# Kernel optimization log

Hardware: AMD Instinct MI355X
Metric: run time of the kernel (lower is better)

Reference implementation:

```python
import jax, jax.numpy as jnp
import numpy as np

B = 4        # samples
GP = 6       # graphs per sample (K*2)
N = 1024     # nodes per graph
DIN = 128    # input feature dim
D = 128      # out_channels
E = 16384    # edges per graph


def setup_inputs() -> dict:
    k = jax.random.split(jax.random.key(0), 10)
    G = B * GP
    s = 0.05
    return {
        "x": jax.random.normal(k[0], (G, N, DIN), jnp.float32),
        "edge_attr": jax.random.uniform(k[1], (G, E, 6), jnp.float32),
        "gcn_W": jax.random.normal(k[2], (4, DIN, D), jnp.float32) * s,
        "gcn_b": jnp.zeros((4, D), jnp.float32),
        "Ws": jax.random.normal(k[3], (4, D, D), jnp.float32) * s,
        "lin1_W": jax.random.normal(k[4], (GP * D, 20), jnp.float32) * s,
        "lin1_b": jnp.zeros((20,), jnp.float32),
        "codefc_W": jax.random.normal(k[5], (20, 2), jnp.float32) * s,
        "codefc_b": jnp.zeros((2,), jnp.float32),
        "lin2_W": jax.random.normal(k[6], (GP * D, GP), jnp.float32) * s,
        "lin2_b": jnp.zeros((GP,), jnp.float32),
        "simfc_W": jax.random.normal(k[7], (GP, 2), jnp.float32) * s,
        "simfc_b": jnp.zeros((2,), jnp.float32),
        "edge_index": jax.random.randint(k[8], (G, 2, E), 0, N, jnp.int64),
    }


def _gcn(x, src, dst, ew, W, b):
    # PyG GCNConv with normalize=True, add_self_loops=True (self-loop weight 1)
    n = x.shape[0]
    deg = jax.ops.segment_sum(ew, dst, num_segments=n) + 1.0
    dinv = jax.lax.rsqrt(deg)
    xw = x @ W
    norm = dinv[src] * ew * dinv[dst]               # [E]
    agg = jax.ops.segment_sum(norm[:, None] * xw[src], dst, num_segments=n)
    return agg + (dinv * dinv)[:, None] * xw + b    # self-loop term + bias


def _gnnlayer(x, ei, ea, gcn_W, gcn_b, Ws):
    # x_tmp = sum_i relu(GCN_i(x, ew=edge_attr[:, i+2])) @ Ws[i]
    src, dst = ei[0], ei[1]
    def chan(W, b, Wmix, ew):
        return jnp.maximum(_gcn(x, src, dst, ew, W, b), 0.0) @ Wmix
    return jax.vmap(chan)(gcn_W, gcn_b, Ws, ea[:, 2:6].T).sum(0)  # [N, D]


def _forward(x, edge_attr, gcn_W, gcn_b, Ws, lin1_W, lin1_b, codefc_W,
             codefc_b, lin2_W, lin2_b, simfc_W, simfc_b, edge_index):
    # per-graph GNN layer over all G = B*GP graphs
    x_tmp = jax.vmap(lambda xg, eig, eag: _gnnlayer(xg, eig, eag, gcn_W, gcn_b, Ws))(
        x, edge_index, edge_attr)                    # [G, N, D]
    g = x_tmp.mean(axis=1).reshape(B, GP * D)        # g_matrix [B, 768]
    # L2-normalize rows (F.normalize eps=1e-12)
    xn = x_tmp / jnp.clip(jnp.linalg.norm(x_tmp, axis=-1, keepdims=True), 1e-12)
    xn = xn.reshape(B, GP, N, D)
    # all-pairs cosine sim -> tanh -> 21-bin histogram on [-1, 1] -> weighted sum
    S = jnp.tanh(jnp.einsum('bind,bjmd->bijnm', xn, xn))   # [B,GP,GP,N,N]
    idx = jnp.clip(jnp.floor((S + 1.0) * (21.0 / 2.0)).astype(jnp.int32), 0, 20)
    centers = jnp.linspace(-1.0, 1.0, 21, dtype=jnp.float32)
    # hist/(N*N) dot centers == mean of per-element bin centers
    sim = centers[idx].mean(axis=(3, 4))             # [B, GP, GP]
    # backnet
    feat = jnp.maximum(g @ lin1_W + lin1_b, 0.0)     # feature_of_G [B, 20]
    code = jax.nn.log_softmax(feat @ codefc_W + codefc_b, axis=1)
    strength = g @ lin2_W + lin2_b                   # [B, GP]
    sim_res = jax.nn.log_softmax((sim.mean(axis=2) * strength) @ simfc_W + simfc_b, axis=1)
    r = 0.4 * code + 0.6 * sim_res
    return r, feat


def reference(x, edge_attr, gcn_W, gcn_b, Ws, lin1_W, lin1_b, codefc_W,
              codefc_b, lin2_W, lin2_b, simfc_W, simfc_b, edge_index):
    return _forward(x, edge_attr, gcn_W, gcn_b, Ws, lin1_W, lin1_b, codefc_W,
                    codefc_b, lin2_W, lin2_b, simfc_W, simfc_b, edge_index)
```

## Files before the change

### kernel.cpp

```cpp
#include <hip/hip_runtime.h>

#define NG 24
#define NB 4
#define GPg 6
#define NN 1024
#define DD 128
#define EE 16384

typedef __bf16 bf16;
typedef __bf16 bf16x8 __attribute__((ext_vector_type(8)));
typedef float f32x4 __attribute__((ext_vector_type(4)));

#define GLOBAL_AS __attribute__((address_space(1)))
#define LDS_AS __attribute__((address_space(3)))

__device__ __forceinline__ int binidx(float v) {
  float u = v * v;
  float q = fmaf(fmaf(fmaf(-0.261093f, u, 1.222977f), u, -3.463278f), u, 10.49874f);
  return (int)fmaf(v, q, 10.5f);
}

__global__ void k_histw(const int* __restrict__ ei, int* __restrict__ counts,
                        const float* __restrict__ gW, const float* __restrict__ Ws,
                        bf16* __restrict__ gwt, bf16* __restrict__ wst) {
  int bid = blockIdx.x;
  if (bid >= 1536) {
    int i = (bid - 1536) * 256 + threadIdx.x;
    int c = i >> 14, k = (i >> 7) & 127, j = i & 127;
    gwt[(c << 14) | (j << 7) | k] = (bf16)gW[i];
    wst[(j << 9) | (c << 7) | k] = (bf16)Ws[i];
    return;
  }
  int t = bid * 256 + threadIdx.x;
  int g = t >> 14, e = t & (EE - 1);
  int dst = ei[g * 2 * EE + EE + e];
  atomicAdd(&counts[g * NN + dst], 1);
}

__global__ void k_scan(const int* __restrict__ counts, int* __restrict__ offs,
                       int* __restrict__ cursor) {
  __shared__ int sh[NN];
  int g = blockIdx.x, t = threadIdx.x;
  int myc = counts[g * NN + t];
  sh[t] = myc;
  __syncthreads();
  for (int d2 = 1; d2 < NN; d2 <<= 1) {
    int v = (t >= d2) ? sh[t - d2] : 0;
    __syncthreads();
    sh[t] += v;
    __syncthreads();
  }
  int incl = sh[t];
  int excl = incl - myc;
  offs[g * 1025 + t] = excl;
  cursor[g * NN + t] = excl;
  if (t == NN - 1) offs[g * 1025 + NN] = incl;
}

__global__ void k_scatter(const int* __restrict__ ei, const float* __restrict__ ea,
                          int* __restrict__ cursor, int* __restrict__ csrs,
                          float* __restrict__ csre) {
  int t = blockIdx.x * 256 + threadIdx.x;
  if (t >= NG * EE) return;
  int g = t >> 14, e = t & (EE - 1);
  int src = ei[g * 2 * EE + e], dst = ei[g * 2 * EE + EE + e];
  int pos = atomicAdd(&cursor[g * NN + dst], 1);
  size_t idx = (size_t)g * EE + pos;
  csrs[idx] = src;
  const float* p = ea + ((size_t)g * EE + e) * 6;
  float2 q0 = *(const float2*)(p + 2);
  float2 q1 = *(const float2*)(p + 4);
  f32x4 v; v[0] = q0.x; v[1] = q0.y; v[2] = q1.x; v[3] = q1.y;
  *(f32x4*)(csre + idx * 4) = v;
}

__global__ void k_deg(const int* __restrict__ offs, const float* __restrict__ csre,
                      float* __restrict__ dinv4) {
  int t = blockIdx.x * 256 + threadIdx.x;
  int c = t & 3, n = (t >> 2) & (NN - 1), g = t >> 12;
  int beg = offs[g * 1025 + n], end = offs[g * 1025 + n + 1];
  const float* ep = csre + (size_t)g * EE * 4 + c;
  float s = 1.0f;
  for (int p = beg; p < end; ++p) s += ep[(size_t)p * 4];
  dinv4[t] = rsqrtf(s);
}

__global__ __launch_bounds__(256) void k_xw(const float* __restrict__ x,
                                            const bf16* __restrict__ gwt,
                                            const float* __restrict__ dinv4,
                                            bf16* __restrict__ xw) {
  int bid = blockIdx.x;
  int gc = bid >> 3, mb = bid & 7;
  int g = gc >> 2, c = gc & 3;
  int lane = threadIdx.x & 63, wid = threadIdx.x >> 6;
  int wm = wid >> 1, wn = wid & 1;
  int row0 = mb * 128 + wm * 64, col0 = wn * 64;
  const float* A = x + (size_t)g * NN * DD;
  const bf16* Bt = gwt + (size_t)c * DD * DD;
  int lr = lane & 15, lk = (lane >> 4) * 8;
  f32x4 acc[4][4] = {};
  for (int kc = 0; kc < 128; kc += 32) {
    bf16x8 a[4], b[4];
#pragma unroll
    for (int i2 = 0; i2 < 4; i2++) {
      const f32x4* pa = (const f32x4*)(A + (size_t)(row0 + i2 * 16 + lr) * DD + kc + lk);
      f32x4 f0 = pa[0], f1 = pa[1];
#pragma unroll
      for (int q = 0; q < 4; q++) { a[i2][q] = (bf16)f0[q]; a[i2][4 + q] = (bf16)f1[q]; }
    }
#pragma unroll
    for (int j2 = 0; j2 < 4; j2++)
      b[j2] = *(const bf16x8*)(Bt + (size_t)(col0 + j2 * 16 + lr) * DD + kc + lk);
#pragma unroll
    for (int i2 = 0; i2 < 4; i2++)
#pragma unroll
      for (int j2 = 0; j2 < 4; j2++)
        acc[i2][j2] = __builtin_amdgcn_mfma_f32_16x16x32_bf16(a[i2], b[j2], acc[i2][j2], 0, 0, 0);
  }
  bf16* out = xw + (size_t)g * NN * 512 + c * 128;
  const float* dv = dinv4 + ((size_t)g * NN) * 4 + c;
  int cr = (lane >> 4) * 4, cc = lane & 15;
#pragma unroll
  for (int i2 = 0; i2 < 4; i2++)
#pragma unroll
    for (int r2 = 0; r2 < 4; r2++) {
      int row = row0 + i2 * 16 + cr + r2;
      float dvv = dv[row * 4];
#pragma unroll
      for (int j2 = 0; j2 < 4; j2++)
        out[(size_t)row * 512 + col0 + j2 * 16 + cc] = (bf16)(acc[i2][j2][r2] * dvv);
    }
}

__global__ __launch_bounds__(256) void k_agg(const int* __restrict__ offs, const int* __restrict__ csrs,
                                             const float* __restrict__ csre, const float* __restrict__ dinv4,
                                             const float* __restrict__ gb, const bf16* __restrict__ xw,
                                             bf16* __restrict__ hb) {
  int bid = blockIdx.x;
  int lb = (bid & 7) * (NG * 256 / 8) + (bid >> 3);
  int g = lb >> 8, n4 = lb & 255;
  int wid = threadIdx.x >> 6, lane = threadIdx.x & 63;
  int n = n4 * 4 + wid;
  int c = lane >> 4, d0 = (lane & 15) * 8;
  const bf16* xwg = xw + (size_t)g * NN * 512;
  int beg = offs[g * 1025 + n], end = offs[g * 1025 + n + 1];
  const int* sp = csrs + (size_t)g * EE;
  const float* ep = csre + (size_t)g * EE * 4;
  float dvn = dinv4[((size_t)g * NN + n) * 4 + c];
  float acc[8] = {};
  int p = beg;
  for (; p + 3 < end; p += 4) {
    int s0 = sp[p], s1 = sp[p + 1], s2 = sp[p + 2], s3 = sp[p + 3];
    float w0 = ep[(size_t)p * 4 + c];
    float w1 = ep[(size_t)(p + 1) * 4 + c];
    float w2 = ep[(size_t)(p + 2) * 4 + c];
    float w3 = ep[(size_t)(p + 3) * 4 + c];
    bf16x8 v0 = *(const bf16x8*)(xwg + (size_t)s0 * 512 + lane * 8);
    bf16x8 v1 = *(const bf16x8*)(xwg + (size_t)s1 * 512 + lane * 8);
    bf16x8 v2 = *(const bf16x8*)(xwg + (size_t)s2 * 512 + lane * 8);
    bf16x8 v3 = *(const bf16x8*)(xwg + (size_t)s3 * 512 + lane * 8);
#pragma unroll
    for (int q = 0; q < 8; q++)
      acc[q] += w0 * (float)v0[q] + w1 * (float)v1[q] + w2 * (float)v2[q] + w3 * (float)v3[q];
  }
  for (; p < end; ++p) {
    int s0 = sp[p];
    float w0 = ep[(size_t)p * 4 + c];
    bf16x8 v0 = *(const bf16x8*)(xwg + (size_t)s0 * 512 + lane * 8);
#pragma unroll
    for (int q = 0; q < 8; q++) acc[q] += w0 * (float)v0[q];
  }
  bf16x8 vs = *(const bf16x8*)(xwg + (size_t)n * 512 + lane * 8);
  bf16x8 o;
#pragma unroll
  for (int q = 0; q < 8; q++) {
    float r2 = dvn * (acc[q] + (float)vs[q]) + gb[c * 128 + d0 + q];
    o[q] = (bf16)fmaxf(r2, 0.f);
  }
  *(bf16x8*)(hb + ((size_t)g * NN + n) * 512 + lane * 8) = o;
}

__global__ __launch_bounds__(256) void k_mixn(const bf16* __restrict__ hb,
                                              const bf16* __restrict__ wst,
                                              float* __restrict__ gmat,
                                              bf16* __restrict__ xn) {
  __shared__ float rowssq[128];
  int bid = blockIdx.x;
  int g = bid >> 3, mb = bid & 7;
  int lane = threadIdx.x & 63, wid = threadIdx.x >> 6;
  int wm = wid >> 1, wn = wid & 1;
  int row0 = mb * 128 + wm * 64, col0 = wn * 64;
  const bf16* H = hb + (size_t)g * NN * 512;
  int lr = lane & 15, lk = (lane >> 4) * 8;
  if (threadIdx.x < 128) rowssq[threadIdx.x] = 0.f;
  f32x4 acc[4][4] = {};
  for (int kc = 0; kc < 512; kc += 32) {
    bf16x8 a[4], b[4];
#pragma unroll
    for (int i2 = 0; i2 < 4; i2++)
      a[i2] = *(const bf16x8*)(H + (size_t)(row0 + i2 * 16 + lr) * 512 + kc + lk);
#pragma unroll
    for (int j2 = 0; j2 < 4; j2++)
      b[j2] = *(const bf16x8*)(wst + (size_t)(col0 + j2 * 16 + lr) * 512 + kc + lk);
#pragma unroll
    for (int i2 = 0; i2 < 4; i2++)
#pragma unroll
      for (int j2 = 0; j2 < 4; j2++)
        acc[i2][j2] = __builtin_amdgcn_mfma_f32_16x16x32_bf16(a[i2], b[j2], acc[i2][j2], 0, 0, 0);
  }
  __syncthreads();
  int cr = (lane >> 4) * 4, cc = lane & 15;
#pragma unroll
  for (int i2 = 0; i2 < 4; i2++)
#pragma unroll
    for (int r2 = 0; r2 < 4; r2++) {
      float s = 0.f;
#pragma unroll
      for (int j2 = 0; j2 < 4; j2++) { float v = acc[i2][j2][r2]; s += v * v; }
#pragma unroll
      for (int d2 = 1; d2 < 16; d2 <<= 1) s += __shfl_xor(s, d2);
      if (cc == 0) atomicAdd(&rowssq[wm * 64 + i2 * 16 + cr + r2], s);
    }
#pragma unroll
  for (int j2 = 0; j2 < 4; j2++) {
    float s = 0.f;
#pragma unroll
    for (int i2 = 0; i2 < 4; i2++)
#pragma unroll
      for (int r2 = 0; r2 < 4; r2++) s += acc[i2][j2][r2];
    s += __shfl_xor(s, 16);
    s += __shfl_xor(s, 32);
    if ((lane >> 4) == 0)
      atomicAdd(&gmat[(g / GPg) * 768 + (g % GPg) * 128 + col0 + j2 * 16 + cc], s * (1.0f / NN));
  }
  __syncthreads();
  bf16* xp = xn + (size_t)g * NN * DD;
#pragma unroll
  for (int i2 = 0; i2 < 4; i2++)
#pragma unroll
    for (int r2 = 0; r2 < 4; r2++) {
      int rowl = wm * 64 + i2 * 16 + cr + r2;
      float inv = 1.0f / fmaxf(sqrtf(rowssq[rowl]), 1e-12f);
#pragma unroll
      for (int j2 = 0; j2 < 4; j2++)
        xp[(size_t)(mb * 128 + rowl) * DD + col0 + j2 * 16 + cc] = (bf16)(acc[i2][j2][r2] * inv);
    }
}

__global__ __launch_bounds__(256, 4) void k_pair(const bf16* __restrict__ xn,
                                                 unsigned* __restrict__ simsum) {
  __shared__ char lds[16384];
  int bid = blockIdx.x;
  int lb = (bid & 7) * 168 + (bid >> 3);
  int b = lb / 336, rem = lb % 336;
  int pj = rem >> 4, rem2 = rem & 15;
  int s128 = rem2 >> 1, half = rem2 & 1;
  int r = pj, i = 0;
  while (r >= 6 - i) { r -= 6 - i; ++i; }
  int j = i + r;
  bool isdiag = (i == j);
  int tb = half * 16, te = tb + 16;
  if (isdiag && 4 * s128 > tb) tb = 4 * s128;
  if (tb >= te) return;
  int lane = threadIdx.x & 63, wid = threadIdx.x >> 6;
  int lr = lane & 15, hi16 = (lane >> 4) * 16;
  const char* Ag = (const char*)(xn + ((size_t)(b * GPg + i) * NN + s128 * 128 + wid * 32) * DD);
  const char* Bg0 = (const char*)(xn + (size_t)(b * GPg + j) * NN * DD);

  bf16x8 a[2][4];
#pragma unroll
  for (int g2 = 0; g2 < 2; g2++)
#pragma unroll
    for (int kc = 0; kc < 4; kc++) {
      a[g2][kc] = *(const bf16x8*)(Ag + (g2 * 16 + lr) * 256 + kc * 64 + hi16);
      asm volatile("" :: "v"(a[g2][kc]));
    }

  auto stage = [&](int buf, int tn) {
    const char* src = Bg0 + tn * 8192;
#pragma unroll
    for (int j2 = 0; j2 < 2; ++j2)
      __builtin_amdgcn_global_load_lds(
          (const GLOBAL_AS void*)(src + (j2 * 16 + lr) * 256 + wid * 64 + hi16),
          (LDS_AS void*)(lds + buf * 8192 + wid * 2048 + j2 * 1024), 16, 0, 0);
  };
  stage(0, tb);
  if (tb + 1 < te) stage(1, tb + 1);

  int cnt = 0;
  int cc = lane & 15, cr = (lane >> 4) * 4;
  for (int t = tb; t < te; ++t) {
    int cur = (t - tb) & 1;
    if (t < te - 1) asm volatile("s_waitcnt vmcnt(2)" ::: "memory");
    else            asm volatile("s_waitcnt vmcnt(0)" ::: "memory");
    __builtin_amdgcn_s_barrier();
    const char* Bl = lds + cur * 8192;
    f32x4 acc[2][2] = {};
#pragma unroll
    for (int kc = 0; kc < 4; kc++) {
      bf16x8 bb[2];
#pragma unroll
      for (int j2 = 0; j2 < 2; j2++)
        bb[j2] = *(const bf16x8*)(Bl + kc * 2048 + j2 * 1024 + lane * 16);
#pragma unroll
      for (int g2 = 0; g2 < 2; g2++)
#pragma unroll
        for (int j2 = 0; j2 < 2; j2++)
          acc[g2][j2] = __builtin_amdgcn_mfma_f32_16x16x32_bf16(a[g2][kc], bb[j2], acc[g2][j2], 0, 0, 0);
    }
    asm volatile("s_waitcnt lgkmcnt(0)" ::: "memory");
    __builtin_amdgcn_sched_barrier(0);
    __builtin_amdgcn_s_barrier();
    if (t + 2 < te) stage(cur, t + 2);
    if (isdiag && t < 4 * s128 + 4) {
      int tc = 0;
#pragma unroll
      for (int g2 = 0; g2 < 2; g2++)
#pragma unroll
        for (int j2 = 0; j2 < 2; j2++)
#pragma unroll
          for (int r2 = 0; r2 < 4; r2++) {
            int idx = binidx(acc[g2][j2][r2]);
            int lm = t * 32 + j2 * 16 + cc;
            int ln = s128 * 128 + wid * 32 + g2 * 16 + cr + r2;
            tc += (lm > ln) ? 2 * idx : (lm == ln ? idx : 0);
          }
      cnt += tc;
    } else {
      int tc = 0;
#pragma unroll
      for (int g2 = 0; g2 < 2; g2++)
#pragma unroll
        for (int j2 = 0; j2 < 2; j2++)
#pragma unroll
          for (int r2 = 0; r2 < 4; r2++)
            tc += binidx(acc[g2][j2][r2]);
      cnt += isdiag ? 2 * tc : tc;
    }
  }
#pragma unroll
  for (int d2 = 32; d2; d2 >>= 1) cnt += __shfl_xor(cnt, d2);
  if (lane == 0) atomicAdd(&simsum[((size_t)b * GPg + i) * GPg + j], (unsigned)cnt);
}

__global__ void k_back(const float* __restrict__ gmat, const unsigned* __restrict__ simsum,
                       const float* __restrict__ l1W, const float* __restrict__ l1b,
                       const float* __restrict__ cfW, const float* __restrict__ cfb,
                       const float* __restrict__ l2W, const float* __restrict__ l2b,
                       const float* __restrict__ sfW, const float* __restrict__ sfb,
                       float* __restrict__ out) {
  __shared__ float feat[NB][20];
  __shared__ float strength[NB][GPg];
  __shared__ float simmean[NB][GPg];
  int t = threadIdx.x, g = t >> 3, l = t & 7;
  if (g < 80) {
    int b = g / 20, jj = g % 20;
    float s = 0.f;
#pragma unroll 8
    for (int k = l; k < 768; k += 8) s += gmat[b * 768 + k] * l1W[k * 20 + jj];
    s += __shfl_xor(s, 1); s += __shfl_xor(s, 2); s += __shfl_xor(s, 4);
    if (l == 0) {
      float f = fmaxf(s + l1b[jj], 0.f);
      feat[b][jj] = f;
      out[8 + b * 20 + jj] = f;
    }
  } else if (g < 104) {
    int q = g - 80, b = q / GPg, pp = q % GPg;
    float s = 0.f;
#pragma unroll 8
    for (int k = l; k < 768; k += 8) s += gmat[b * 768 + k] * l2W[k * GPg + pp];
    s += __shfl_xor(s, 1); s += __shfl_xor(s, 2); s += __shfl_xor(s, 4);
    if (l == 0) strength[b][pp] = s + l2b[pp];
  } else if (t >= 832 && t < 856) {
    int q = t - 832; int b = q / GPg, ii = q % GPg;
    float s = 0.f;
    for (int jj = 0; jj < GPg; jj++) {
      int lo = ii < jj ? ii : jj, hi = ii < jj ? jj : ii;
      s += -1.0f + 0.1f * (float)simsum[(b * GPg + lo) * GPg + hi] * (1.0f / (1024.f * 1024.f));
    }
    simmean[b][ii] = s * (1.0f / GPg);
  }
  __syncthreads();
  if (t < NB) {
    int b = t;
    float l1v[2], l2v[2];
#pragma unroll
    for (int u = 0; u < 2; u++) {
      float s = cfb[u];
      for (int jj = 0; jj < 20; jj++) s += feat[b][jj] * cfW[jj * 2 + u];
      l1v[u] = s;
      float s2 = sfb[u];
      for (int pp = 0; pp < GPg; pp++) s2 += simmean[b][pp] * strength[b][pp] * sfW[pp * 2 + u];
      l2v[u] = s2;
    }
    float m1 = fmaxf(l1v[0], l1v[1]);
    float lse1 = m1 + logf(expf(l1v[0] - m1) + expf(l1v[1] - m1));
    float m2 = fmaxf(l2v[0], l2v[1]);
    float lse2 = m2 + logf(expf(l2v[0] - m2) + expf(l2v[1] - m2));
    out[b * 2 + 0] = 0.4f * (l1v[0] - lse1) + 0.6f * (l2v[0] - lse2);
    out[b * 2 + 1] = 0.4f * (l1v[1] - lse1) + 0.6f * (l2v[1] - lse2);
  }
}

extern "C" void kernel_launch(void* const* d_in, const int* in_sizes, int n_in,
                              void* d_out, int out_size, void* d_ws, size_t ws_size,
                              hipStream_t stream) {
  const float* x   = (const float*)d_in[0];
  const float* ea  = (const float*)d_in[1];
  const float* gW  = (const float*)d_in[2];
  const float* gb  = (const float*)d_in[3];
  const float* Ws  = (const float*)d_in[4];
  const float* l1W = (const float*)d_in[5];
  const float* l1b = (const float*)d_in[6];
  const float* cfW = (const float*)d_in[7];
  const float* cfb = (const float*)d_in[8];
  const float* l2W = (const float*)d_in[9];
  const float* l2b = (const float*)d_in[10];
  const float* sfW = (const float*)d_in[11];
  const float* sfb = (const float*)d_in[12];
  const int* eidx  = (const int*)d_in[13];
  float* out = (float*)d_out;

  char* w = (char*)d_ws;
  auto alloc = [&](size_t bytes) { char* p = w; w += (bytes + 255) & ~(size_t)255; return (void*)p; };
  bf16* gwt     = (bf16*)alloc(4 * DD * DD * 2);
  bf16* wst     = (bf16*)alloc(4 * DD * DD * 2);
  int* counts   = (int*)alloc((size_t)NG * NN * 4);
  float* dinv4  = (float*)alloc((size_t)NG * NN * 4 * 4);
  int* offs     = (int*)alloc((size_t)NG * 1025 * 4);
  int* cursor   = (int*)alloc((size_t)NG * NN * 4);
  int* csrs     = (int*)alloc((size_t)NG * EE * 4);
  float* csre   = (float*)alloc((size_t)NG * EE * 4 * 4);
  bf16* xw      = (bf16*)alloc((size_t)NG * NN * 512 * 2);
  bf16* hb      = (bf16*)alloc((size_t)NG * NN * 512 * 2);
  float* gmat   = (float*)alloc((size_t)NB * 768 * 4);
  unsigned* simsum = (unsigned*)alloc((size_t)NB * 36 * 4);
  bf16* xn      = (bf16*)alloc((size_t)NG * NN * DD * 2);

  hipMemsetAsync(counts, 0, (size_t)NG * NN * 4, stream);
  hipMemsetAsync(gmat, 0, 12288 + 576, stream);

  k_histw<<<1792, 256, 0, stream>>>(eidx, counts, gW, Ws, gwt, wst);
  k_scan<<<NG, 1024, 0, stream>>>(counts, offs, cursor);
  k_scatter<<<(NG * EE) / 256, 256, 0, stream>>>(eidx, ea, cursor, csrs, csre);
  k_deg<<<(NG * NN * 4) / 256, 256, 0, stream>>>(offs, csre, dinv4);
  k_xw<<<NG * 4 * 8, 256, 0, stream>>>(x, gwt, dinv4, xw);
  k_agg<<<NG * 256, 256, 0, stream>>>(offs, csrs, csre, dinv4, gb, xw, hb);
  k_mixn<<<NG * 8, 256, 0, stream>>>(hb, wst, gmat, xn);
  k_pair<<<1344, 256, 0, stream>>>(xn, simsum);
  k_back<<<1, 1024, 0, stream>>>(gmat, simsum, l1W, l1b, cfW, cfb, l2W, l2b, sfW, sfb, out);
}
```

Measured before the change: 181.0 us.

## Use wave-shuffle scan, merge memsets, and raise occupancy hints on agg/pair

The block scan is rebuilt from a shared-memory Hillis-Steele loop with many barriers into a wavefront shuffle scan followed by a small scan over per-wave sums. The workspace is reordered so counts, gmat and simsum sit next to each other, which lets one memset clear all three instead of two separate calls. Launch bounds for k_agg and k_pair are raised to ask for more waves per SIMD, which may force register spilling. The gmat/simsum memset size still relies on 256-byte alloc rounding leaving the buffers contiguous.

```diff
diff --git a/kernel.cpp b/kernel.cpp
--- a/kernel.cpp
+++ b/kernel.cpp
@@ -39,18 +39,29 @@
 
 __global__ void k_scan(const int* __restrict__ counts, int* __restrict__ offs,
                        int* __restrict__ cursor) {
-  __shared__ int sh[NN];
+  __shared__ int wsum[16];
   int g = blockIdx.x, t = threadIdx.x;
+  int lane = t & 63, wv = t >> 6;
   int myc = counts[g * NN + t];
-  sh[t] = myc;
+  int v = myc;
+#pragma unroll
+  for (int d = 1; d < 64; d <<= 1) {
+    int u = __shfl_up(v, d);
+    if (lane >= d) v += u;
+  }
+  if (lane == 63) wsum[wv] = v;
   __syncthreads();
-  for (int d2 = 1; d2 < NN; d2 <<= 1) {
-    int v = (t >= d2) ? sh[t - d2] : 0;
-    __syncthreads();
-    sh[t] += v;
-    __syncthreads();
-  }
-  int incl = sh[t];
+  if (t < 16) {
+    int s = wsum[t];
+#pragma unroll
+    for (int d = 1; d < 16; d <<= 1) {
+      int u = __shfl_up(s, d);
+      if (t >= d) s += u;
+    }
+    wsum[t] = s;
+  }
+  __syncthreads();
+  int incl = v + (wv > 0 ? wsum[wv - 1] : 0);
   int excl = incl - myc;
   offs[g * 1025 + t] = excl;
   cursor[g * NN + t] = excl;
@@ -132,10 +143,10 @@
     }
 }
 
-__global__ __launch_bounds__(256) void k_agg(const int* __restrict__ offs, const int* __restrict__ csrs,
-                                             const float* __restrict__ csre, const float* __restrict__ dinv4,
-                                             const float* __restrict__ gb, const bf16* __restrict__ xw,
-                                             bf16* __restrict__ hb) {
+__global__ __launch_bounds__(256, 8) void k_agg(const int* __restrict__ offs, const int* __restrict__ csrs,
+                                                const float* __restrict__ csre, const float* __restrict__ dinv4,
+                                                const float* __restrict__ gb, const bf16* __restrict__ xw,
+                                                bf16* __restrict__ hb) {
   int bid = blockIdx.x;
   int lb = (bid & 7) * (NG * 256 / 8) + (bid >> 3);
   int g = lb >> 8, n4 = lb & 255;
@@ -247,7 +258,7 @@
     }
 }
 
-__global__ __launch_bounds__(256, 4) void k_pair(const bf16* __restrict__ xn,
+__global__ __launch_bounds__(256, 6) void k_pair(const bf16* __restrict__ xn,
                                                  unsigned* __restrict__ simsum) {
   __shared__ char lds[16384];
   int bid = blockIdx.x;
@@ -426,6 +437,8 @@
   bf16* gwt     = (bf16*)alloc(4 * DD * DD * 2);
   bf16* wst     = (bf16*)alloc(4 * DD * DD * 2);
   int* counts   = (int*)alloc((size_t)NG * NN * 4);
+  float* gmat   = (float*)alloc((size_t)NB * 768 * 4);
+  unsigned* simsum = (unsigned*)alloc((size_t)NB * 36 * 4);
   float* dinv4  = (float*)alloc((size_t)NG * NN * 4 * 4);
   int* offs     = (int*)alloc((size_t)NG * 1025 * 4);
   int* cursor   = (int*)alloc((size_t)NG * NN * 4);
@@ -433,12 +446,9 @@
   float* csre   = (float*)alloc((size_t)NG * EE * 4 * 4);
   bf16* xw      = (bf16*)alloc((size_t)NG * NN * 512 * 2);
   bf16* hb      = (bf16*)alloc((size_t)NG * NN * 512 * 2);
-  float* gmat   = (float*)alloc((size_t)NB * 768 * 4);
-  unsigned* simsum = (unsigned*)alloc((size_t)NB * 36 * 4);
   bf16* xn      = (bf16*)alloc((size_t)NG * NN * DD * 2);
 
-  hipMemsetAsync(counts, 0, (size_t)NG * NN * 4, stream);
-  hipMemsetAsync(gmat, 0, 12288 + 576, stream);
+  hipMemsetAsync(counts, 0, (size_t)NG * NN * 4 + 12288 + 576, stream);
 
   k_histw<<<1792, 256, 0, stream>>>(eidx, counts, gW, Ws, gwt, wst);
   k_scan<<<NG, 1024, 0, stream>>>(counts, offs, cursor);
```

Measured after the change: 223.0 us. 23.2% more time.
